# Kernel tuning notes

Hardware: AMD Instinct MI355X
Metric: run time of the kernel (lower is better)

Reference implementation:

```python
import jax, jax.numpy as jnp
import numpy as np

H, W = 512, 512
FEAT_LEVELS = [3, 4, 5, 6, 7]
NEG_THRESH, POS_THRESH = 0.4, 0.5
N_GT = 1024


def make_priors():
    """Prior boxes in cxcywh, same order as the torch itertools.product loops."""
    out = []
    for lvl in FEAT_LEVELS:
        s = 2 ** lvl
        ys = np.arange(s // 2, H, s, dtype=np.float32)
        xs = np.arange(s // 2, W, s, dtype=np.float32)
        cy, cx = np.meshgrid(ys, xs, indexing='ij')          # row-major over (cy, cx)
        centers = np.stack([cx.ravel(), cy.ravel()], axis=-1)  # [C, 2] = (cx, cy)
        wh = []
        for aspect in [0.5, 1.0, 2.0]:
            for scale in [0.0, 1.0 / 3.0, 2.0 / 3.0]:
                h = 4 * s * (2.0 ** scale) * np.sqrt(aspect)
                w = 4 * s * (2.0 ** scale) / np.sqrt(aspect)
                wh.append([w, h])
        wh = np.asarray(wh, np.float32)                       # [9, 2]
        C = centers.shape[0]
        cxy = np.repeat(centers, 9, axis=0)                   # [C*9, 2]
        whr = np.tile(wh, (C, 1))                             # [C*9, 2]
        out.append(np.concatenate([cxy, whr], axis=-1))
    return np.concatenate(out, axis=0).astype(np.float32)     # [M, 4]


def cxcywh_to_xyxy(b):
    cx, cy, w, h = b[..., 0], b[..., 1], b[..., 2], b[..., 3]
    return jnp.stack([cx - w / 2, cy - h / 2, cx + w / 2, cy + h / 2], axis=-1)


def xyxy_to_cxcywh(b):
    x1, y1, x2, y2 = b[..., 0], b[..., 1], b[..., 2], b[..., 3]
    return jnp.stack([(x1 + x2) / 2, (y1 + y2) / 2, x2 - x1, y2 - y1], axis=-1)


def box_iou(a, b):
    # a: [N,4], b: [M,4] (xyxy) -> [N,M]
    area_a = (a[:, 2] - a[:, 0]) * (a[:, 3] - a[:, 1])
    area_b = (b[:, 2] - b[:, 0]) * (b[:, 3] - b[:, 1])
    lt = jnp.maximum(a[:, None, :2], b[None, :, :2])   # [N,M,2]
    rb = jnp.minimum(a[:, None, 2:], b[None, :, 2:])
    wh = jnp.clip(rb - lt, 0.0)
    inter = wh[..., 0] * wh[..., 1]
    return inter / (area_a[:, None] + area_b[None, :] - inter)


def setup_inputs() -> dict:
    key = jax.random.key(0)
    k1, k2, k3, k4 = jax.random.split(key, 4)
    cx = jax.random.uniform(k1, (N_GT,), jnp.float32, 16.0, float(W) - 16.0)
    cy = jax.random.uniform(k2, (N_GT,), jnp.float32, 16.0, float(H) - 16.0)
    wh = jax.random.uniform(k3, (N_GT, 2), jnp.float32, 8.0, 256.0)
    bboxes = jnp.stack([cx - wh[:, 0] / 2, cy - wh[:, 1] / 2,
                        cx + wh[:, 0] / 2, cy + wh[:, 1] / 2], axis=-1)
    labels = jax.random.randint(k4, (N_GT,), 1, 81, dtype=jnp.int64 if jax.config.jax_enable_x64 else jnp.int32)
    priors = jnp.asarray(make_priors())
    return {"bboxes": bboxes, "labels": labels, "priors": priors}


def reference(bboxes, labels, priors):
    n = bboxes.shape[0]
    ious = box_iou(bboxes, cxcywh_to_xyxy(priors))          # [N, M]
    max_ious = ious.max(axis=0)                             # [M]
    match_ids = ious.argmax(axis=0)                         # [M]
    force_assign_ids = ious.argmax(axis=1)                  # [N]
    match_ids = match_ids.at[force_assign_ids].set(jnp.arange(n))
    max_ious = max_ious.at[force_assign_ids].set(POS_THRESH)

    matched = xyxy_to_cxcywh(bboxes)[match_ids]             # [M, 4]
    dcx = (matched[..., 0] - priors[..., 0]) / priors[..., 2] / 0.1
    dcy = (matched[..., 1] - priors[..., 1]) / priors[..., 3] / 0.1
    dw = jnp.log(matched[..., 2] / priors[..., 2]) / 0.2
    dh = jnp.log(matched[..., 3] / priors[..., 3]) / 0.2
    reg_targets = jnp.stack([dcx, dcy, dw, dh], axis=-1)    # [M, 4]

    cls_targets = labels[match_ids]
    cls_targets = jnp.where(max_ious < POS_THRESH, -1, cls_targets)
    cls_targets = jnp.where(max_ious < NEG_THRESH, 0, cls_targets)
    return reg_targets, cls_targets
```

## Files before the change

kernel.cpp:

```cpp
#include <hip/hip_runtime.h>


static constexpr float NEG_THRESH = 0.4f;
static constexpr float POS_THRESH = 0.5f;
static constexpr int N_GT = 1024;
static constexpr int GT_PER_BLK = 64;
static constexpr int NCHUNK = N_GT / GT_PER_BLK;
static constexpr int MPAD = 49152;
static constexpr int BLK = 256;
static constexpr int NB = MPAD / BLK;
static constexpr int T_ROWS = 16;
static constexpr int STRIDE = 264;

__device__ __forceinline__ unsigned long long packiou(float iou, unsigned idx_) {
    return ((unsigned long long)__float_as_uint(iou) << 32) |
           (unsigned long long)(0xFFFFFFFFu - idx_);
}

__global__ void __launch_bounds__(256) fused_kernel(
        const float* __restrict__ bboxes,
        const float* __restrict__ priors,
        unsigned long long* __restrict__ part1,
        unsigned long long* __restrict__ partG,
        int* __restrict__ force_n,
        int M) {
#pragma clang fp contract(off)
    __shared__ float tile[T_ROWS][STRIDE];
    __shared__ float sgx1[GT_PER_BLK], sgy1[GT_PER_BLK];
    __shared__ float sgx2[GT_PER_BLK], sgy2[GT_PER_BLK], sgar[GT_PER_BLK];
    __shared__ unsigned short sidx[GT_PER_BLK];
    __shared__ float sbb[4][4];
    __shared__ int scount;

    int tid = threadIdx.x;
    int lane = tid & 63;
    int wid = tid >> 6;
    int bx = (NB - 1) - blockIdx.y;
    int n0 = blockIdx.x * GT_PER_BLK;
    int m = bx * BLK + tid;
    bool valid = (m < M);

    float4 p = valid ? reinterpret_cast<const float4*>(priors)[m]
                     : make_float4(0.f, 0.f, 0.f, 0.f);
    float bx1 = p.x - p.z / 2.0f;
    float by1 = p.y - p.w / 2.0f;
    float bx2 = p.x + p.z / 2.0f;
    float by2 = p.y + p.w / 2.0f;
    float area_b = (bx2 - bx1) * (by2 - by1);

    float mnx = valid ? bx1 : 1e30f;
    float mny = valid ? by1 : 1e30f;
    float mxx = valid ? bx2 : -1e30f;
    float mxy = valid ? by2 : -1e30f;
#pragma unroll
    for (int mk = 1; mk < 64; mk <<= 1) {
        mnx = fminf(mnx, __shfl_xor(mnx, mk));
        mny = fminf(mny, __shfl_xor(mny, mk));
        mxx = fmaxf(mxx, __shfl_xor(mxx, mk));
        mxy = fmaxf(mxy, __shfl_xor(mxy, mk));
    }
    if (lane == 0) {
        sbb[wid][0] = mnx; sbb[wid][1] = mny; sbb[wid][2] = mxx; sbb[wid][3] = mxy;
    }
    __syncthreads();

    if (tid < 64) {
        float BX1 = fminf(fminf(sbb[0][0], sbb[1][0]), fminf(sbb[2][0], sbb[3][0]));
        float BY1 = fminf(fminf(sbb[0][1], sbb[1][1]), fminf(sbb[2][1], sbb[3][1]));
        float BX2 = fmaxf(fmaxf(sbb[0][2], sbb[1][2]), fmaxf(sbb[2][2], sbb[3][2]));
        float BY2 = fmaxf(fmaxf(sbb[0][3], sbb[1][3]), fmaxf(sbb[2][3], sbb[3][3]));
        float4 g = reinterpret_cast<const float4*>(bboxes)[n0 + tid];
        bool hit = (g.x < BX2) & (g.z > BX1) & (g.y < BY2) & (g.w > BY1);
        unsigned long long bal = __ballot(hit);
        if (hit) {
            int pos = __popcll(bal & ((1ull << tid) - 1ull));
            sgx1[pos] = g.x; sgy1[pos] = g.y;
            sgx2[pos] = g.z; sgy2[pos] = g.w;
            sgar[pos] = (g.z - g.x) * (g.w - g.y);
            sidx[pos] = (unsigned short)tid;
        }
        if (tid == 0) scount = __popcll(bal);
    }
    __syncthreads();
    int cnt = scount;

    float best = 0.0f;
    int bestn = n0;

    int row = tid >> 4;
    int sub = tid & 15;
    int m0 = bx * BLK;

    int nfull = cnt >> 4;
    int tail = cnt & 15;

    for (int b = 0; b <= nfull; ++b) {
        int rows = (b < nfull) ? T_ROWS : tail;
        if (rows == 0) break;
        int base = b * T_ROWS;

#pragma unroll
        for (int r = 0; r < T_ROWS; ++r) {
            if (r < rows) {
                int idx = base + r;
                float gx1 = sgx1[idx], gy1 = sgy1[idx];
                float gx2 = sgx2[idx], gy2 = sgy2[idx];
                float ga  = sgar[idx];
                int   jn  = n0 + (int)sidx[idx];

                float ltx = fmaxf(gx1, bx1);
                float lty = fmaxf(gy1, by1);
                float rbx = fminf(gx2, bx2);
                float rby = fminf(gy2, by2);
                float w = rbx - ltx; if (w < 0.0f) w = 0.0f;
                float h = rby - lty; if (h < 0.0f) h = 0.0f;
                float inter = w * h;
                float iou = inter / (ga + area_b - inter);

                if (iou > best) { best = iou; bestn = jn; }
                tile[r][tid] = valid ? iou : -1.0f;
            } else {
                tile[r][tid] = -1.0f;
            }
        }
        __syncthreads();

        float bi = -2.0f;
        int bm = 0;
#pragma unroll
        for (int k = 0; k < BLK / 16; ++k) {
            int col = sub + 16 * k;
            float v = tile[row][col];
            if (v > bi) { bi = v; bm = col; }
        }
#pragma unroll
        for (int msk = 1; msk < 16; msk <<= 1) {
            float oi = __shfl_xor(bi, msk);
            int om = __shfl_xor(bm, msk);
            if (oi > bi || (oi == bi && om < bm)) { bi = oi; bm = om; }
        }
        if (sub == 0 && bi > 0.0f) {
            int jr = (int)sidx[base + row];
            atomicMax(&partG[n0 + jr], packiou(bi, (unsigned)(m0 + bm)));
        }
        __syncthreads();
    }

    if (valid) {
        atomicMax(&part1[m], packiou(best, (unsigned)bestn));
        if (blockIdx.x == 0) force_n[m] = -1;
    }
}

__global__ void rs_kernel(const unsigned long long* __restrict__ partG,
                          int* __restrict__ force_n) {
    int n = blockIdx.x * blockDim.x + threadIdx.x;
    if (n >= N_GT) return;
    unsigned long long v = partG[n];
    int m = (int)(0xFFFFFFFFu - (unsigned)(v & 0xFFFFFFFFull));
    atomicMax(&force_n[m], n);
}

__global__ void __launch_bounds__(256) encode_kernel(
        const float* __restrict__ bboxes,
        const int* __restrict__ labels,
        const float* __restrict__ priors,
        const unsigned long long* __restrict__ part1,
        const int* __restrict__ force_n,
        float* __restrict__ out, int M) {
#pragma clang fp contract(off)
    int m = blockIdx.x * 256 + threadIdx.x;
    if (m >= M) return;

    unsigned long long v = part1[m];
    float iou = __uint_as_float((unsigned)(v >> 32));
    int mid = (int)(0xFFFFFFFFu - (unsigned)(v & 0xFFFFFFFFull));

    int f = force_n[m];
    if (f >= 0) { mid = f; iou = POS_THRESH; }

    float4 g = reinterpret_cast<const float4*>(bboxes)[mid];
    float mcx = (g.x + g.z) / 2.0f;
    float mcy = (g.y + g.w) / 2.0f;
    float mw = g.z - g.x;
    float mh = g.w - g.y;

    float4 p = reinterpret_cast<const float4*>(priors)[m];
    float dcx = ((mcx - p.x) / p.z) / 0.1f;
    float dcy = ((mcy - p.y) / p.w) / 0.1f;
    float dw = logf(mw / p.z) / 0.2f;
    float dh = logf(mh / p.w) / 0.2f;

    reinterpret_cast<float4*>(out)[m] = make_float4(dcx, dcy, dw, dh);

    int cls = labels[mid];
    if (iou < POS_THRESH) cls = -1;
    if (iou < NEG_THRESH) cls = 0;
    out[(size_t)4 * M + m] = (float)cls;
}

extern "C" void kernel_launch(void* const* d_in, const int* in_sizes, int n_in,
                              void* d_out, int out_size, void* d_ws, size_t ws_size,
                              hipStream_t stream) {
    const float* bboxes = (const float*)d_in[0];
    const int* labels = (const int*)d_in[1];
    const float* priors = (const float*)d_in[2];
    int M = in_sizes[2] / 4;
    float* out = (float*)d_out;

    char* ws = (char*)d_ws;
    unsigned long long* part1 = (unsigned long long*)ws;
    unsigned long long* partG = (unsigned long long*)(ws + (size_t)MPAD * 8);
    int* force_n = (int*)(ws + (size_t)MPAD * 8 + (size_t)N_GT * 8);

    hipMemsetAsync(part1, 0, (size_t)(MPAD + N_GT) * 8, stream);

    fused_kernel<<<dim3(NCHUNK, NB), 256, 0, stream>>>(bboxes, priors, part1,
                                                       partG, force_n, M);
    rs_kernel<<<(N_GT + 255) / 256, 256, 0, stream>>>(partG, force_n);
    encode_kernel<<<(MPAD + 255) / 256, 256, 0, stream>>>(bboxes, labels, priors,
                                                          part1, force_n, out, M);
}
```

Baseline: 38.38 us.

## Replace global atomics with per-chunk partial buffers and two priors per thread

Each thread now handles two priors (512 per block), and the gt box data is packed into float4/float2 shared arrays. The global atomicMax calls on part1 and partG are replaced by plain stores into per-chunk partial arrays, which the rs and encode kernels then reduce by scanning. This also removes the memset. The cost is more workspace and extra serial reduction loops in rs_kernel (NB=96 reads per gt) and encode_kernel (16 reads per prior).

```diff
diff --git a/kernel.cpp b/kernel.cpp
--- a/kernel.cpp
+++ b/kernel.cpp
@@ -7,10 +7,10 @@
 static constexpr int GT_PER_BLK = 64;
 static constexpr int NCHUNK = N_GT / GT_PER_BLK;
 static constexpr int MPAD = 49152;
-static constexpr int BLK = 256;
+static constexpr int BLK = 512;
 static constexpr int NB = MPAD / BLK;
-static constexpr int T_ROWS = 16;
-static constexpr int STRIDE = 264;
+static constexpr int T_ROWS = 8;
+static constexpr int STRIDE = 520;
 
 __device__ __forceinline__ unsigned long long packiou(float iou, unsigned idx_) {
     return ((unsigned long long)__float_as_uint(iou) << 32) |
@@ -20,38 +20,45 @@
 __global__ void __launch_bounds__(256) fused_kernel(
         const float* __restrict__ bboxes,
         const float* __restrict__ priors,
-        unsigned long long* __restrict__ part1,
-        unsigned long long* __restrict__ partG,
+        unsigned long long* __restrict__ part1c,
+        unsigned long long* __restrict__ partGc,
         int* __restrict__ force_n,
         int M) {
 #pragma clang fp contract(off)
     __shared__ float tile[T_ROWS][STRIDE];
-    __shared__ float sgx1[GT_PER_BLK], sgy1[GT_PER_BLK];
-    __shared__ float sgx2[GT_PER_BLK], sgy2[GT_PER_BLK], sgar[GT_PER_BLK];
-    __shared__ unsigned short sidx[GT_PER_BLK];
+    __shared__ float4 sgbox[GT_PER_BLK];
+    __shared__ float2 sgmeta[GT_PER_BLK];
+    __shared__ unsigned long long swin[GT_PER_BLK];
     __shared__ float sbb[4][4];
     __shared__ int scount;
 
     int tid = threadIdx.x;
     int lane = tid & 63;
     int wid = tid >> 6;
-    int bx = (NB - 1) - blockIdx.y;
-    int n0 = blockIdx.x * GT_PER_BLK;
-    int m = bx * BLK + tid;
-    bool valid = (m < M);
-
-    float4 p = valid ? reinterpret_cast<const float4*>(priors)[m]
-                     : make_float4(0.f, 0.f, 0.f, 0.f);
-    float bx1 = p.x - p.z / 2.0f;
-    float by1 = p.y - p.w / 2.0f;
-    float bx2 = p.x + p.z / 2.0f;
-    float by2 = p.y + p.w / 2.0f;
-    float area_b = (bx2 - bx1) * (by2 - by1);
-
-    float mnx = valid ? bx1 : 1e30f;
-    float mny = valid ? by1 : 1e30f;
-    float mxx = valid ? bx2 : -1e30f;
-    float mxy = valid ? by2 : -1e30f;
+    int cx = blockIdx.x;
+    int by = (NB - 1) - blockIdx.y;
+    int n0 = cx * GT_PER_BLK;
+    int m0 = by * BLK;
+    int mA = m0 + tid;
+    int mB = mA + 256;
+    bool validA = (mA < M);
+    bool validB = (mB < M);
+
+    float4 pA = validA ? reinterpret_cast<const float4*>(priors)[mA]
+                       : make_float4(0.f, 0.f, 0.f, 0.f);
+    float4 pB = validB ? reinterpret_cast<const float4*>(priors)[mB]
+                       : make_float4(0.f, 0.f, 0.f, 0.f);
+    float ax1 = pA.x - pA.z / 2.0f, ay1 = pA.y - pA.w / 2.0f;
+    float ax2 = pA.x + pA.z / 2.0f, ay2 = pA.y + pA.w / 2.0f;
+    float areaA = (ax2 - ax1) * (ay2 - ay1);
+    float bx1 = pB.x - pB.z / 2.0f, by1 = pB.y - pB.w / 2.0f;
+    float bx2 = pB.x + pB.z / 2.0f, by2 = pB.y + pB.w / 2.0f;
+    float areaB = (bx2 - bx1) * (by2 - by1);
+
+    float mnx = validA ? ax1 : 1e30f;  if (validB) mnx = fminf(mnx, bx1);
+    float mny = validA ? ay1 : 1e30f;  if (validB) mny = fminf(mny, by1);
+    float mxx = validA ? ax2 : -1e30f; if (validB) mxx = fmaxf(mxx, bx2);
+    float mxy = validA ? ay2 : -1e30f; if (validB) mxy = fmaxf(mxy, by2);
 #pragma unroll
     for (int mk = 1; mk < 64; mk <<= 1) {
         mnx = fminf(mnx, __shfl_xor(mnx, mk));
@@ -74,25 +81,23 @@
         unsigned long long bal = __ballot(hit);
         if (hit) {
             int pos = __popcll(bal & ((1ull << tid) - 1ull));
-            sgx1[pos] = g.x; sgy1[pos] = g.y;
-            sgx2[pos] = g.z; sgy2[pos] = g.w;
-            sgar[pos] = (g.z - g.x) * (g.w - g.y);
-            sidx[pos] = (unsigned short)tid;
+            sgbox[pos] = g;
+            sgmeta[pos] = make_float2((g.z - g.x) * (g.w - g.y), (float)tid);
         }
         if (tid == 0) scount = __popcll(bal);
+        swin[tid] = 0ull;
     }
     __syncthreads();
     int cnt = scount;
 
-    float best = 0.0f;
-    int bestn = n0;
-
-    int row = tid >> 4;
-    int sub = tid & 15;
-    int m0 = bx * BLK;
-
-    int nfull = cnt >> 4;
-    int tail = cnt & 15;
+    float bestA = 0.0f, bestB = 0.0f;
+    int bestnA = n0, bestnB = n0;
+
+    int row = tid >> 5;
+    int sub = tid & 31;
+
+    int nfull = cnt >> 3;
+    int tail = cnt & 7;
 
     for (int b = 0; b <= nfull; ++b) {
         int rows = (b < nfull) ? T_ROWS : tail;
@@ -103,61 +108,81 @@
         for (int r = 0; r < T_ROWS; ++r) {
             if (r < rows) {
                 int idx = base + r;
-                float gx1 = sgx1[idx], gy1 = sgy1[idx];
-                float gx2 = sgx2[idx], gy2 = sgy2[idx];
-                float ga  = sgar[idx];
-                int   jn  = n0 + (int)sidx[idx];
-
-                float ltx = fmaxf(gx1, bx1);
-                float lty = fmaxf(gy1, by1);
-                float rbx = fminf(gx2, bx2);
-                float rby = fminf(gy2, by2);
+                float4 gb = sgbox[idx];
+                float2 mt = sgmeta[idx];
+                int jn = n0 + (int)mt.y;
+
+                float ltx = fmaxf(gb.x, ax1);
+                float lty = fmaxf(gb.y, ay1);
+                float rbx = fminf(gb.z, ax2);
+                float rby = fminf(gb.w, ay2);
                 float w = rbx - ltx; if (w < 0.0f) w = 0.0f;
                 float h = rby - lty; if (h < 0.0f) h = 0.0f;
                 float inter = w * h;
-                float iou = inter / (ga + area_b - inter);
-
-                if (iou > best) { best = iou; bestn = jn; }
-                tile[r][tid] = valid ? iou : -1.0f;
-            } else {
-                tile[r][tid] = -1.0f;
+                float iouA = inter / (mt.x + areaA - inter);
+
+                float ltx2 = fmaxf(gb.x, bx1);
+                float lty2 = fmaxf(gb.y, by1);
+                float rbx2 = fminf(gb.z, bx2);
+                float rby2 = fminf(gb.w, by2);
+                float w2 = rbx2 - ltx2; if (w2 < 0.0f) w2 = 0.0f;
+                float h2 = rby2 - lty2; if (h2 < 0.0f) h2 = 0.0f;
+                float inter2 = w2 * h2;
+                float iouB = inter2 / (mt.x + areaB - inter2);
+
+                if (iouA > bestA) { bestA = iouA; bestnA = jn; }
+                if (iouB > bestB) { bestB = iouB; bestnB = jn; }
+                tile[r][tid] = validA ? iouA : -1.0f;
+                tile[r][tid + 256] = validB ? iouB : -1.0f;
             }
         }
         __syncthreads();
 
-        float bi = -2.0f;
-        int bm = 0;
-#pragma unroll
-        for (int k = 0; k < BLK / 16; ++k) {
-            int col = sub + 16 * k;
-            float v = tile[row][col];
-            if (v > bi) { bi = v; bm = col; }
-        }
-#pragma unroll
-        for (int msk = 1; msk < 16; msk <<= 1) {
-            float oi = __shfl_xor(bi, msk);
-            int om = __shfl_xor(bm, msk);
-            if (oi > bi || (oi == bi && om < bm)) { bi = oi; bm = om; }
-        }
-        if (sub == 0 && bi > 0.0f) {
-            int jr = (int)sidx[base + row];
-            atomicMax(&partG[n0 + jr], packiou(bi, (unsigned)(m0 + bm)));
+        if (row < rows) {
+            float bi = -2.0f;
+            int bm = 0;
+#pragma unroll
+            for (int k = 0; k < BLK / 32; ++k) {
+                int col = sub + 32 * k;
+                float v = tile[row][col];
+                if (v > bi) { bi = v; bm = col; }
+            }
+#pragma unroll
+            for (int msk = 1; msk < 32; msk <<= 1) {
+                float oi = __shfl_xor(bi, msk);
+                int om = __shfl_xor(bm, msk);
+                if (oi > bi || (oi == bi && om < bm)) { bi = oi; bm = om; }
+            }
+            if (sub == 0 && bi > 0.0f) {
+                int jr = (int)sgmeta[base + row].y;
+                swin[jr] = packiou(bi, (unsigned)(m0 + bm));
+            }
         }
         __syncthreads();
     }
 
-    if (valid) {
-        atomicMax(&part1[m], packiou(best, (unsigned)bestn));
-        if (blockIdx.x == 0) force_n[m] = -1;
-    }
-}
-
-__global__ void rs_kernel(const unsigned long long* __restrict__ partG,
+    if (tid < GT_PER_BLK) {
+        partGc[(size_t)by * N_GT + n0 + tid] = swin[tid];
+    }
+    size_t rowc = (size_t)cx * MPAD;
+    if (validA) part1c[rowc + mA] = packiou(bestA, (unsigned)bestnA);
+    if (validB) part1c[rowc + mB] = packiou(bestB, (unsigned)bestnB);
+    if (cx == 0) {
+        if (validA) force_n[mA] = -1;
+        if (validB) force_n[mB] = -1;
+    }
+}
+
+__global__ void rs_kernel(const unsigned long long* __restrict__ partGc,
                           int* __restrict__ force_n) {
     int n = blockIdx.x * blockDim.x + threadIdx.x;
     if (n >= N_GT) return;
-    unsigned long long v = partG[n];
-    int m = (int)(0xFFFFFFFFu - (unsigned)(v & 0xFFFFFFFFull));
+    unsigned long long best = 0ull;
+    for (int c = 0; c < NB; ++c) {
+        unsigned long long v = partGc[(size_t)c * N_GT + n];
+        if (v > best) best = v;
+    }
+    int m = (int)(0xFFFFFFFFu - (unsigned)(best & 0xFFFFFFFFull));
     atomicMax(&force_n[m], n);
 }
 
@@ -165,16 +190,20 @@
         const float* __restrict__ bboxes,
         const int* __restrict__ labels,
         const float* __restrict__ priors,
-        const unsigned long long* __restrict__ part1,
+        const unsigned long long* __restrict__ part1c,
         const int* __restrict__ force_n,
         float* __restrict__ out, int M) {
 #pragma clang fp contract(off)
     int m = blockIdx.x * 256 + threadIdx.x;
     if (m >= M) return;
 
-    unsigned long long v = part1[m];
-    float iou = __uint_as_float((unsigned)(v >> 32));
-    int mid = (int)(0xFFFFFFFFu - (unsigned)(v & 0xFFFFFFFFull));
+    unsigned long long best = part1c[m];
+    for (int c = 1; c < NCHUNK; ++c) {
+        unsigned long long v = part1c[(size_t)c * MPAD + m];
+        if (v > best) best = v;
+    }
+    float iou = __uint_as_float((unsigned)(best >> 32));
+    int mid = (int)(0xFFFFFFFFu - (unsigned)(best & 0xFFFFFFFFull));
 
     int f = force_n[m];
     if (f >= 0) { mid = f; iou = POS_THRESH; }
@@ -209,15 +238,15 @@
     float* out = (float*)d_out;
 
     char* ws = (char*)d_ws;
-    unsigned long long* part1 = (unsigned long long*)ws;
-    unsigned long long* partG = (unsigned long long*)(ws + (size_t)MPAD * 8);
-    int* force_n = (int*)(ws + (size_t)MPAD * 8 + (size_t)N_GT * 8);
-
-    hipMemsetAsync(part1, 0, (size_t)(MPAD + N_GT) * 8, stream);
-
-    fused_kernel<<<dim3(NCHUNK, NB), 256, 0, stream>>>(bboxes, priors, part1,
-                                                       partG, force_n, M);
-    rs_kernel<<<(N_GT + 255) / 256, 256, 0, stream>>>(partG, force_n);
+    unsigned long long* part1c = (unsigned long long*)ws;
+    unsigned long long* partGc =
+        (unsigned long long*)(ws + (size_t)NCHUNK * MPAD * 8);
+    int* force_n =
+        (int*)(ws + (size_t)NCHUNK * MPAD * 8 + (size_t)NB * N_GT * 8);
+
+    fused_kernel<<<dim3(NCHUNK, NB), 256, 0, stream>>>(bboxes, priors, part1c,
+                                                       partGc, force_n, M);
+    rs_kernel<<<(N_GT + 255) / 256, 256, 0, stream>>>(partGc, force_n);
     encode_kernel<<<(MPAD + 255) / 256, 256, 0, stream>>>(bboxes, labels, priors,
-                                                          part1, force_n, out, M);
-}
+                                                          part1c, force_n, out, M);
+}
```

New measurement: 45.88 us. 1.2x slower.
